# Kernel tuning notes

Hardware: AMD Instinct MI355X
Metric: run time of the kernel (lower is better)

Reference implementation:

```python
import jax, jax.numpy as jnp
from jax import lax
import numpy as np

B, N, D = 8, 4096, 64
S = 1024          # groups
K = 32            # kneighbors
RADIUS = 0.2


def farthest_point_sample(xyz, npoint):
    """xyz: [B,N,3] -> centroid indices [B,npoint]. Deterministic start at index 0
    (original torch uses a random start index)."""
    b, n, _ = xyz.shape

    def step(carry, _):
        distance, farthest = carry                              # [B,N], [B]
        centroid = jnp.take_along_axis(xyz, farthest[:, None, None], axis=1)  # [B,1,3]
        dist = jnp.sum((xyz - centroid) ** 2, axis=-1)          # [B,N]
        distance = jnp.minimum(distance, dist)
        new_far = jnp.argmax(distance, axis=-1)
        return (distance, new_far), farthest

    init = (jnp.full((b, n), 1e10, xyz.dtype), jnp.zeros((b,), jnp.int32))
    _, cents = lax.scan(step, init, None, length=npoint)        # [npoint,B]
    return cents.T                                              # [B,npoint]


def square_distance(src, dst):
    # [B,N,M] squared euclidean distances
    d = -2.0 * jnp.einsum('bnc,bmc->bnm', src, dst)
    d += jnp.sum(src ** 2, -1)[:, :, None]
    d += jnp.sum(dst ** 2, -1)[:, None, :]
    return d


def query_ball_point(radius, nsample, xyz, new_xyz):
    b, n, _ = xyz.shape
    s = new_xyz.shape[1]
    sqrdists = square_distance(new_xyz, xyz)                    # [B,S,N]
    arange = jnp.arange(n, dtype=jnp.int32)[None, None, :]
    group_idx = jnp.where(sqrdists > radius ** 2, n, arange)    # [B,S,N]
    group_idx = jnp.sort(group_idx, axis=-1)[:, :, :nsample]    # [B,S,K]
    first = group_idx[:, :, :1]
    group_idx = jnp.where(group_idx == n, first, group_idx)
    return group_idx


def gather_points(points, idx):
    # points [B,N,C], idx [B,...] -> [B,...,C]
    return jax.vmap(lambda p, i: p[i])(points, idx)


def setup_inputs() -> dict:
    key = jax.random.key(0)
    k1, k2 = jax.random.split(key)
    xyz = jax.random.uniform(k1, (B, N, 3), dtype=jnp.float32)
    points = jax.random.normal(k2, (B, N, D), dtype=jnp.float32)
    return {"xyz": xyz, "points": points}


def reference(xyz, points):
    fps_idx = farthest_point_sample(xyz, S)                     # [B,S]
    new_xyz = gather_points(xyz, fps_idx)                       # [B,S,3]
    anchor_feat = gather_points(points, fps_idx)                # [B,S,D]
    idx = query_ball_point(RADIUS, K, xyz, new_xyz)             # [B,S,K]
    grouped_xyz = gather_points(xyz, idx)                       # [B,S,K,3]
    grouped_points = gather_points(points, idx)                 # [B,S,K,D]
    grouped_points = jnp.concatenate([grouped_points, grouped_xyz], axis=-1)  # use_xyz
    anchor_rep = jnp.broadcast_to(anchor_feat[:, :, None, :], (B, S, K, D))
    new_points = jnp.concatenate([grouped_points, anchor_rep], axis=-1)  # [B,S,K,2D+3]
    return new_xyz, new_points
```

## Files before the change

kernel.cpp:

```cpp
#include <hip/hip_runtime.h>

#define BB 8
#define NN 4096
#define DD 64
#define SS 1024
#define KK 32
#define R2 0.04f

#define DPP_STAGE(p, CTRL)                                                            \
    {                                                                                 \
        unsigned _lo = (unsigned)(p), _hi = (unsigned)((p) >> 32);                    \
        unsigned _olo = (unsigned)__builtin_amdgcn_update_dpp((int)_lo, (int)_lo,     \
                                                              CTRL, 0xf, 0xf, false); \
        unsigned _ohi = (unsigned)__builtin_amdgcn_update_dpp((int)_hi, (int)_hi,     \
                                                              CTRL, 0xf, 0xf, false); \
        unsigned long long _o = ((unsigned long long)_ohi << 32) | _olo;              \
        if (_o > (p)) (p) = _o;                                                       \
    }

__global__ __launch_bounds__(512) void fps_kernel(const float* __restrict__ xyz,
                                                  int* __restrict__ fps_idx) {
    __shared__ float sx[NN], sy[NN], sz[NN];
    __shared__ unsigned long long red[2][8];

    const int b   = blockIdx.x;
    const int tid = threadIdx.x;
    const float* xb = xyz + (size_t)b * NN * 3;

    float px[8], py[8], pz[8], dist[8];
#pragma unroll
    for (int j = 0; j < 8; ++j) {
        const int i = tid + 512 * j;
        const float x = xb[i * 3 + 0];
        const float y = xb[i * 3 + 1];
        const float z = xb[i * 3 + 2];
        px[j] = x; py[j] = y; pz[j] = z;
        sx[i] = x; sy[i] = y; sz[i] = z;
        dist[j] = 1e10f;
    }
    __syncthreads();

    int far = 0;
    for (int t = 0; t < SS; ++t) {
        if (tid == 0) fps_idx[b * SS + t] = far;
        const float cx = sx[far], cy = sy[far], cz = sz[far];

        float bestv = -1.0f;
        int   bestj = 0;
#pragma unroll
        for (int j = 0; j < 8; ++j) {
            const float dx = __fsub_rn(px[j], cx);
            const float dy = __fsub_rn(py[j], cy);
            const float dz = __fsub_rn(pz[j], cz);
            const float d  = __fadd_rn(__fadd_rn(__fmul_rn(dx, dx), __fmul_rn(dy, dy)),
                                       __fmul_rn(dz, dz));
            const float nd = fminf(dist[j], d);
            dist[j] = nd;
            if (nd > bestv) { bestv = nd; bestj = j; }
        }
        const int besti = tid + 512 * bestj;
        unsigned long long p =
            ((unsigned long long)__float_as_uint(bestv) << 32) | (unsigned)(~besti);

        DPP_STAGE(p, 0x111);
        DPP_STAGE(p, 0x112);
        DPP_STAGE(p, 0x114);
        DPP_STAGE(p, 0x118);
        DPP_STAGE(p, 0x142);
        DPP_STAGE(p, 0x143);

        const int par = t & 1;
        if ((tid & 63) == 63) red[par][tid >> 6] = p;
        __syncthreads();
        unsigned long long m = red[par][0];
#pragma unroll
        for (int w = 1; w < 8; ++w) {
            const unsigned long long o = red[par][w];
            if (o > m) m = o;
        }
        far = (int)(~(unsigned)m);
    }
}

__global__ __launch_bounds__(256) void ball_kernel(const float* __restrict__ xyz,
                                                   const int* __restrict__ fps_idx,
                                                   int* __restrict__ ball_idx) {
    __shared__ int buf[4][KK];
    const int wave = threadIdx.x >> 6;
    const int lane = threadIdx.x & 63;
    const int gw   = blockIdx.x * 4 + wave;
    const int b    = gw / SS;
    const float* xb = xyz + (size_t)b * NN * 3;

    const int   qi = fps_idx[gw];
    const float qx = xb[qi * 3 + 0], qy = xb[qi * 3 + 1], qz = xb[qi * 3 + 2];
    const float qn = __fadd_rn(__fadd_rn(__fmul_rn(qx, qx), __fmul_rn(qy, qy)),
                               __fmul_rn(qz, qz));

    int total = 0;
    for (int base = 0; base < NN && total < KK; base += 64) {
        const int n  = base + lane;
        const float px = xb[n * 3 + 0], py = xb[n * 3 + 1], pz = xb[n * 3 + 2];
        const float pn = __fadd_rn(__fadd_rn(__fmul_rn(px, px), __fmul_rn(py, py)),
                                   __fmul_rn(pz, pz));
        const float dt = __fadd_rn(__fadd_rn(__fmul_rn(qx, px), __fmul_rn(qy, py)),
                                   __fmul_rn(qz, pz));
        const float d = __fadd_rn(__fadd_rn(__fmul_rn(-2.0f, dt), qn), pn);
        const bool hit = !(d > R2);
        const unsigned long long mask = __ballot(hit);
        const int before = __popcll(mask & ((1ull << lane) - 1ull));
        const int pos = total + before;
        if (hit && pos < KK) buf[wave][pos] = n;
        total += (int)__popcll(mask);
    }
    __syncthreads();
    if (lane < KK) {
        const int v = (lane < total) ? buf[wave][lane] : buf[wave][0];
        ball_idx[gw * KK + lane] = v;
    }
}

__global__ __launch_bounds__(256) void write_kernel(const float* __restrict__ xyz,
                                                    const float* __restrict__ points,
                                                    const int* __restrict__ fps_idx,
                                                    const int* __restrict__ ball_idx,
                                                    float* __restrict__ out) {
    const int bs = blockIdx.x;
    const int b  = bs / SS;
    __shared__ int   sidx[KK];
    __shared__ float sanchor[DD];
    __shared__ int   sq;
    const int tid = threadIdx.x;

    if (tid < KK) sidx[tid] = ball_idx[bs * KK + tid];
    if (tid == 0) sq = fps_idx[bs];
    __syncthreads();
    const int qi = sq;
    const float* xb = xyz + (size_t)b * NN * 3;
    const float* pb = points + (size_t)b * NN * DD;
    if (tid < DD) sanchor[tid] = pb[qi * DD + tid];
    if (tid < 3)  out[(size_t)bs * 3 + tid] = xb[qi * 3 + tid];
    __syncthreads();

    float* outp = out + (size_t)BB * SS * 3 + (size_t)bs * KK * 131;
    for (int c = tid; c < KK * 131; c += 256) {
        const int k = c / 131;
        const int j = c - k * 131;
        const int idx = sidx[k];
        float v;
        if (j < DD)          v = pb[idx * DD + j];
        else if (j < DD + 3) v = xb[idx * 3 + (j - DD)];
        else                 v = sanchor[j - DD - 3];
        outp[c] = v;
    }
}

extern "C" void kernel_launch(void* const* d_in, const int* in_sizes, int n_in,
                              void* d_out, int out_size, void* d_ws, size_t ws_size,
                              hipStream_t stream) {
    const float* xyz    = (const float*)d_in[0];
    const float* points = (const float*)d_in[1];
    float* out = (float*)d_out;

    int* fps  = (int*)d_ws;
    int* ball = fps + BB * SS;

    fps_kernel<<<BB, 512, 0, stream>>>(xyz, fps);
    ball_kernel<<<(BB * SS) / 4, 256, 0, stream>>>(xyz, fps, ball);
    write_kernel<<<BB * SS, 256, 0, stream>>>(xyz, points, fps, ball, out);
}
```

Measured before the change: 828.0 us.

## Vectorize FPS distance update and reduce argmax with float-only DPP max

Each thread now owns 8 contiguous points loaded with float4 reads and kept as packed float2 vectors, so distance updates can use packed FP32 math. The per-wave argmax reduction switches from 64-bit value/index DPP pairs to a float-only DPP max, then recovers the winning index with a ballot, find-first-set and readlane. Contiguous indexing per thread keeps the lowest-index tie-break while halving the DPP traffic in the serial 1024-step loop. It adds a ballot/readlane step and relies on exact float equality to find the winner.

```diff
diff --git a/kernel.cpp b/kernel.cpp
--- a/kernel.cpp
+++ b/kernel.cpp
@@ -7,19 +7,18 @@
 #define KK 32
 #define R2 0.04f
 
-#define DPP_STAGE(p, CTRL)                                                            \
-    {                                                                                 \
-        unsigned _lo = (unsigned)(p), _hi = (unsigned)((p) >> 32);                    \
-        unsigned _olo = (unsigned)__builtin_amdgcn_update_dpp((int)_lo, (int)_lo,     \
-                                                              CTRL, 0xf, 0xf, false); \
-        unsigned _ohi = (unsigned)__builtin_amdgcn_update_dpp((int)_hi, (int)_hi,     \
-                                                              CTRL, 0xf, 0xf, false); \
-        unsigned long long _o = ((unsigned long long)_ohi << 32) | _olo;              \
-        if (_o > (p)) (p) = _o;                                                       \
+typedef float f32x2 __attribute__((ext_vector_type(2)));
+
+#define DPP_MAXF(wv, CTRL)                                                             \
+    {                                                                                  \
+        int _o = __builtin_amdgcn_update_dpp(__float_as_int(wv), __float_as_int(wv),   \
+                                             CTRL, 0xf, 0xf, false);                   \
+        (wv) = fmaxf((wv), __int_as_float(_o));                                        \
     }
 
 __global__ __launch_bounds__(512) void fps_kernel(const float* __restrict__ xyz,
                                                   int* __restrict__ fps_idx) {
+#pragma clang fp contract(off)
     __shared__ float sx[NN], sy[NN], sz[NN];
     __shared__ unsigned long long red[2][8];
 
@@ -27,16 +26,22 @@
     const int tid = threadIdx.x;
     const float* xb = xyz + (size_t)b * NN * 3;
 
-    float px[8], py[8], pz[8], dist[8];
+    const float4* xb4 = (const float4*)(xb + tid * 24);
+    const float4 q0 = xb4[0], q1 = xb4[1], q2 = xb4[2];
+    const float4 q3 = xb4[3], q4 = xb4[4], q5 = xb4[5];
+
+    f32x2 px[4], py[4], pz[4], dist[4];
+    px[0] = (f32x2){q0.x, q0.w}; py[0] = (f32x2){q0.y, q1.x}; pz[0] = (f32x2){q0.z, q1.y};
+    px[1] = (f32x2){q1.z, q2.y}; py[1] = (f32x2){q1.w, q2.z}; pz[1] = (f32x2){q2.x, q2.w};
+    px[2] = (f32x2){q3.x, q3.w}; py[2] = (f32x2){q3.y, q4.x}; pz[2] = (f32x2){q3.z, q4.y};
+    px[3] = (f32x2){q4.z, q5.y}; py[3] = (f32x2){q4.w, q5.z}; pz[3] = (f32x2){q5.x, q5.w};
 #pragma unroll
-    for (int j = 0; j < 8; ++j) {
-        const int i = tid + 512 * j;
-        const float x = xb[i * 3 + 0];
-        const float y = xb[i * 3 + 1];
-        const float z = xb[i * 3 + 2];
-        px[j] = x; py[j] = y; pz[j] = z;
-        sx[i] = x; sy[i] = y; sz[i] = z;
-        dist[j] = 1e10f;
+    for (int jj = 0; jj < 4; ++jj) {
+        const int i0 = tid * 8 + 2 * jj;
+        sx[i0] = px[jj].x; sx[i0 + 1] = px[jj].y;
+        sy[i0] = py[jj].x; sy[i0 + 1] = py[jj].y;
+        sz[i0] = pz[jj].x; sz[i0 + 1] = pz[jj].y;
+        dist[jj] = (f32x2){1e10f, 1e10f};
     }
     __syncthreads();
 
@@ -44,33 +49,48 @@
     for (int t = 0; t < SS; ++t) {
         if (tid == 0) fps_idx[b * SS + t] = far;
         const float cx = sx[far], cy = sy[far], cz = sz[far];
+        const f32x2 cx2 = (f32x2){cx, cx}, cy2 = (f32x2){cy, cy}, cz2 = (f32x2){cz, cz};
 
-        float bestv = -1.0f;
-        int   bestj = 0;
+        f32x2 nd[4];
 #pragma unroll
-        for (int j = 0; j < 8; ++j) {
-            const float dx = __fsub_rn(px[j], cx);
-            const float dy = __fsub_rn(py[j], cy);
-            const float dz = __fsub_rn(pz[j], cz);
-            const float d  = __fadd_rn(__fadd_rn(__fmul_rn(dx, dx), __fmul_rn(dy, dy)),
-                                       __fmul_rn(dz, dz));
-            const float nd = fminf(dist[j], d);
-            dist[j] = nd;
-            if (nd > bestv) { bestv = nd; bestj = j; }
+        for (int jj = 0; jj < 4; ++jj) {
+            const f32x2 dx = px[jj] - cx2;
+            const f32x2 dy = py[jj] - cy2;
+            const f32x2 dz = pz[jj] - cz2;
+            const f32x2 d  = (dx * dx + dy * dy) + dz * dz;
+            f32x2 m;
+            m.x = fminf(dist[jj].x, d.x);
+            m.y = fminf(dist[jj].y, d.y);
+            dist[jj] = m;
+            nd[jj] = m;
         }
-        const int besti = tid + 512 * bestj;
-        unsigned long long p =
-            ((unsigned long long)__float_as_uint(bestv) << 32) | (unsigned)(~besti);
+        const float bestv = fmaxf(fmaxf(fmaxf(nd[0].x, nd[0].y), fmaxf(nd[1].x, nd[1].y)),
+                                  fmaxf(fmaxf(nd[2].x, nd[2].y), fmaxf(nd[3].x, nd[3].y)));
+        int localj = 0;
+#pragma unroll
+        for (int j = 7; j >= 0; --j) {
+            const float v = (j & 1) ? nd[j >> 1].y : nd[j >> 1].x;
+            if (v == bestv) localj = j;
+        }
 
-        DPP_STAGE(p, 0x111);
-        DPP_STAGE(p, 0x112);
-        DPP_STAGE(p, 0x114);
-        DPP_STAGE(p, 0x118);
-        DPP_STAGE(p, 0x142);
-        DPP_STAGE(p, 0x143);
+        float wv = bestv;
+        DPP_MAXF(wv, 0x111);
+        DPP_MAXF(wv, 0x112);
+        DPP_MAXF(wv, 0x114);
+        DPP_MAXF(wv, 0x118);
+        DPP_MAXF(wv, 0x142);
+        DPP_MAXF(wv, 0x143);
+        const float maxw = __int_as_float(__builtin_amdgcn_readlane(__float_as_int(wv), 63));
 
+        const unsigned long long hits = __ballot(bestv == maxw);
+        const int L = __ffsll((unsigned long long)hits) - 1;
+        const int candv = tid * 8 + localj;
+        const int cand  = __builtin_amdgcn_readlane(candv, L);
+
+        const unsigned long long p =
+            ((unsigned long long)__float_as_uint(maxw) << 32) | (unsigned)(~cand);
         const int par = t & 1;
-        if ((tid & 63) == 63) red[par][tid >> 6] = p;
+        if ((tid & 63) == 0) red[par][tid >> 6] = p;
         __syncthreads();
         unsigned long long m = red[par][0];
 #pragma unroll
```

Measured after the change: 787.0 us. -5.0%, faster.
